# Performance work log

Measured on AMD Instinct MI355X. Metric: run time of the kernel, lower is better.

## Reference

```python
import jax, jax.numpy as jnp
import numpy as np

N = 100000
E = 600000
H = 128
G = 64          # number of graphs
LN_EPS = 1e-5


def setup_inputs() -> dict:
    key = jax.random.key(0)
    ks = jax.random.split(key, 16)
    node = jax.random.normal(ks[0], (N, H), dtype=jnp.float32)
    edge_index = jax.random.randint(ks[1], (2, E), 0, N, dtype=jnp.int64)
    edge_attr = jax.random.normal(ks[2], (E, 1), dtype=jnp.float32)
    batch_ptr = jnp.sort(jax.random.randint(ks[3], (N,), 0, G, dtype=jnp.int64))
    s = 1.0 / np.sqrt(H)
    params = dict(
        eps=jnp.float32(0.0),  # GINConv train_eps=True, init 0
        W1=jax.random.uniform(ks[4], (H, H), jnp.float32, -s, s),
        b1=jnp.zeros((H,), jnp.float32),
        g1=jnp.ones((H,), jnp.float32), be1=jnp.zeros((H,), jnp.float32),
        W2=jax.random.uniform(ks[5], (H, H), jnp.float32, -s, s),
        b2=jnp.zeros((H,), jnp.float32),
        g2=jnp.ones((H,), jnp.float32), be2=jnp.zeros((H,), jnp.float32),
        W3=jax.random.uniform(ks[6], (H, H), jnp.float32, -s, s),
        b3=jnp.zeros((H,), jnp.float32),
        ln_w=jnp.ones((H,), jnp.float32), ln_b=jnp.zeros((H,), jnp.float32),
    )
    return dict(node=node, edge_index=edge_index, edge_attr=edge_attr,
                batch_ptr=batch_ptr, **params)


def _layernorm(x, g, b):
    mu = x.mean(-1, keepdims=True)
    var = ((x - mu) ** 2).mean(-1, keepdims=True)
    return (x - mu) * jax.lax.rsqrt(var + LN_EPS) * g + b


def _forward(node, edge_index, batch_ptr, eps, W1, b1, g1, be1, W2, b2, g2, be2,
             W3, b3, ln_w, ln_b):
    src, dst = edge_index[0], edge_index[1]
    # GIN sum aggregation: scatter-add neighbor features to targets
    agg = jax.ops.segment_sum(node[src], dst, num_segments=N)  # [N, H]
    h = (1.0 + eps) * node + agg
    # 3-layer MLP (PyG MLP: lin -> LayerNorm -> ReLU, final lin plain)
    h = jax.nn.relu(_layernorm(h @ W1 + b1, g1, be1))
    h = jax.nn.relu(_layernorm(h @ W2 + b2, g2, be2))
    h = h @ W3 + b3
    # PyG graph-mode LayerNorm: normalize over all nodes+features per graph
    cnt = jax.ops.segment_sum(jnp.ones((N,), h.dtype), batch_ptr, num_segments=G)
    norm = jnp.maximum(cnt * H, 1.0)                       # [G]
    mean = jax.ops.segment_sum(h.sum(-1), batch_ptr, num_segments=G) / norm
    hc = h - mean[batch_ptr][:, None]
    var = jax.ops.segment_sum((hc * hc).sum(-1), batch_ptr, num_segments=G) / norm
    out = hc * jax.lax.rsqrt(var + LN_EPS)[batch_ptr][:, None] * ln_w + ln_b
    return jax.nn.relu(out)


def reference(node, edge_index, edge_attr, batch_ptr, eps, W1, b1, g1, be1,
              W2, b2, g2, be2, W3, b3, ln_w, ln_b):
    del edge_attr  # accepted by GIN_Layer.forward but unused
    return _forward(node, edge_index, batch_ptr, eps, W1, b1, g1, be1,
                    W2, b2, g2, be2, W3, b3, ln_w, ln_b)
```

## Files before the change

### kernel.cpp

```cpp
#include <hip/hip_runtime.h>

#define N_NODES 100000
#define N_EDGES 600000
#define H 128
#define G_NUM 64
#define LN_EPS 1e-5f

#define WSTR 136

#define NTILES ((N_NODES + 63) / 64)

#define SCAN_CHUNK 1024
#define SCAN_NB ((N_NODES + SCAN_CHUNK - 1) / SCAN_CHUNK)
#define HIST_NB ((N_EDGES + 255) / 256)
#define CVT_NB ((N_NODES * H / 8 + 255) / 256)
#define FILL_NB ((N_EDGES + 255) / 256)
#define WT_NB ((3 * 16384 + 255) / 256)

#define SCR_MAX 272

#define WT_IOFF 900612
#define NBF_IOFF 925192
#define NEEDED_WS ((size_t)NBF_IOFF * 4 + (size_t)N_NODES * H * 2)

typedef __attribute__((ext_vector_type(8))) short short8;
typedef __attribute__((ext_vector_type(4))) float floatx4;

__device__ __forceinline__ unsigned short f2bf(float x) {
    unsigned int u = __float_as_uint(x);
    u += 0x7fffu + ((u >> 16) & 1u);
    return (unsigned short)(u >> 16);
}

__global__ __launch_bounds__(256) void hist_cvt_kernel(
    const int* __restrict__ ei, int* __restrict__ deg,
    const float* __restrict__ node, unsigned int* __restrict__ node_bf)
{
    int gb = blockIdx.x;
    if (gb < HIST_NB) {
        int e = gb * 256 + threadIdx.x;
        if (e >= N_EDGES) return;
        atomicAdd(&deg[ei[N_EDGES + e]], 1);
    } else {
        int i = (gb - HIST_NB) * 256 + threadIdx.x;
        if (i >= N_NODES * H / 8) return;
        float4 a = ((const float4*)node)[i * 2];
        float4 b = ((const float4*)node)[i * 2 + 1];
        uint4 p;
        p.x = (unsigned)f2bf(a.x) | ((unsigned)f2bf(a.y) << 16);
        p.y = (unsigned)f2bf(a.z) | ((unsigned)f2bf(a.w) << 16);
        p.z = (unsigned)f2bf(b.x) | ((unsigned)f2bf(b.y) << 16);
        p.w = (unsigned)f2bf(b.z) | ((unsigned)f2bf(b.w) << 16);
        ((uint4*)node_bf)[i] = p;
    }
}

__global__ __launch_bounds__(256) void scan1_kernel(
    const int* __restrict__ deg, int* __restrict__ off,
    int* __restrict__ blksum)
{
    __shared__ int sA[256], sB[256];
    const int tid = threadIdx.x;
    const int base = blockIdx.x * SCAN_CHUNK + tid * 4;
    int v[4];
#pragma unroll
    for (int j = 0; j < 4; ++j) {
        int i = base + j;
        v[j] = (i < N_NODES) ? deg[i] : 0;
    }
    int tsum = v[0] + v[1] + v[2] + v[3];
    int* a = sA; int* b = sB;
    a[tid] = tsum;
    __syncthreads();
#pragma unroll
    for (int o = 1; o < 256; o <<= 1) {
        int t = a[tid] + ((tid >= o) ? a[tid - o] : 0);
        b[tid] = t;
        __syncthreads();
        int* tmp = a; a = b; b = tmp;
    }
    int run = a[tid] - tsum;
#pragma unroll
    for (int j = 0; j < 4; ++j) {
        int i = base + j;
        if (i < N_NODES) off[i] = run;
        run += v[j];
    }
    if (tid == 255) blksum[blockIdx.x] = a[255];
}

__global__ __launch_bounds__(256) void scan23_kernel(
    int* __restrict__ off, const int* __restrict__ blksum,
    int* __restrict__ cursor)
{
    __shared__ int sA[128], sB[128];
    const int tid = threadIdx.x;
    if (tid < 128) sA[tid] = (tid < SCAN_NB) ? blksum[tid] : 0;
    __syncthreads();
    int* a = sA; int* b = sB;
#pragma unroll
    for (int o = 1; o < 128; o <<= 1) {
        int t = 0;
        if (tid < 128) t = a[tid] + ((tid >= o) ? a[tid - o] : 0);
        __syncthreads();
        if (tid < 128) b[tid] = t;
        __syncthreads();
        int* tmp = a; a = b; b = tmp;
    }
    int excl = 0;
    if (tid < 128) excl = a[tid] - ((tid < SCAN_NB) ? blksum[tid] : 0);
    __syncthreads();
    if (tid < 128) sA[tid] = excl;
    __syncthreads();

    int i = blockIdx.x * 256 + tid;
    if (i < N_NODES) {
        int val = off[i] + sA[i >> 10];
        off[i] = val;
        cursor[i] = val;
    }
    if (i == 0) off[N_NODES] = N_EDGES;
}

__global__ __launch_bounds__(256) void fill_wt_kernel(
    const int* __restrict__ ei, int* __restrict__ cursor,
    int* __restrict__ csr,
    const float* __restrict__ W1, const float* __restrict__ W2,
    const float* __restrict__ W3, unsigned short* __restrict__ WT)
{
    int gb = blockIdx.x;
    if (gb < FILL_NB) {
        int e = gb * 256 + threadIdx.x;
        if (e >= N_EDGES) return;
        int dst = ei[N_EDGES + e];
        int pos = atomicAdd(&cursor[dst], 1);
        csr[pos] = ei[e];
    } else {
        int idx = (gb - FILL_NB) * 256 + threadIdx.x;
        if (idx >= 3 * 16384) return;
        int l = idx >> 14, r = idx & 16383;
        int frag = r >> 3, j = r & 7;
        int lane = frag & 63, ktnt = frag >> 6;
        int kt = ktnt & 3, nt = ktnt >> 2;
        int c = lane & 15, q = lane >> 4;
        int n = nt * 16 + c;
        int k = kt * 32 + q * 8 + j;
        const float* W = (l == 0) ? W1 : ((l == 1) ? W2 : W3);
        WT[l * 16384 + r] = f2bf(W[k * 128 + n]);
    }
}

__device__ __forceinline__ void gemm_frags(const unsigned short* hIn,
                                           const unsigned short* __restrict__ WTl,
                                           floatx4 acc[8], int w, int lane)
{
    const int c = lane & 15, q = lane >> 4;
#pragma unroll
    for (int nt = 0; nt < 8; ++nt) acc[nt] = (floatx4){0.f, 0.f, 0.f, 0.f};
#pragma unroll
    for (int kt = 0; kt < 4; ++kt) {
        short8 a = *(const short8*)&hIn[(w * 16 + c) * WSTR + kt * 32 + q * 8];
#pragma unroll
        for (int nt = 0; nt < 8; ++nt) {
            short8 b = *(const short8*)&WTl[(nt * 256 + kt * 64 + lane) * 8];
            acc[nt] = __builtin_amdgcn_mfma_f32_16x16x32_bf16(a, b, acc[nt], 0, 0, 0);
        }
    }
}

__device__ __forceinline__ void gemm_layer_ln(unsigned short* h,
                                              const unsigned short* __restrict__ WTl,
                                              const float* __restrict__ bias,
                                              const float* __restrict__ g,
                                              const float* __restrict__ be,
                                              int w, int lane)
{
    const int c = lane & 15, q = lane >> 4;
    floatx4 acc[8];
    gemm_frags(h, WTl, acc, w, lane);

    float sum[4] = {0.f, 0.f, 0.f, 0.f};
    float sq[4]  = {0.f, 0.f, 0.f, 0.f};
#pragma unroll
    for (int nt = 0; nt < 8; ++nt) {
        float bv = bias[nt * 16 + c];
#pragma unroll
        for (int i = 0; i < 4; ++i) {
            float vv = acc[nt][i] + bv;
            acc[nt][i] = vv;
            sum[i] += vv; sq[i] += vv * vv;
        }
    }
#pragma unroll
    for (int m = 1; m < 16; m <<= 1) {
#pragma unroll
        for (int i = 0; i < 4; ++i) {
            sum[i] += __shfl_xor(sum[i], m);
            sq[i]  += __shfl_xor(sq[i], m);
        }
    }
    float mu[4], rstd[4];
#pragma unroll
    for (int i = 0; i < 4; ++i) {
        mu[i]   = sum[i] * (1.0f / 128.0f);
        rstd[i] = rsqrtf(sq[i] * (1.0f / 128.0f) - mu[i] * mu[i] + LN_EPS);
    }
#pragma unroll
    for (int nt = 0; nt < 8; ++nt) {
        float gw = g[nt * 16 + c];
        float bw = be[nt * 16 + c];
#pragma unroll
        for (int i = 0; i < 4; ++i) {
            float val = fmaxf(0.f, (acc[nt][i] - mu[i]) * rstd[i] * gw + bw);
            h[(w * 16 + q * 4 + i) * WSTR + nt * 16 + c] = f2bf(val);
        }
    }
}

template <bool NBF>
__global__ __launch_bounds__(256, 6) void fused_mlp_kernel(
    const float* __restrict__ node, const unsigned int* __restrict__ nbf,
    const int* __restrict__ off,
    const int* __restrict__ csr, const float* __restrict__ epsp,
    const unsigned short* __restrict__ WT,
    const float* __restrict__ b1, const float* __restrict__ g1,
    const float* __restrict__ be1,
    const float* __restrict__ b2, const float* __restrict__ g2,
    const float* __restrict__ be2,
    const float* __restrict__ b3, const int* __restrict__ batch,
    float* __restrict__ out, float* __restrict__ gstat)
{
    __shared__ unsigned short hA[64 * WSTR];
    __shared__ float prm[7 * 128];
    __shared__ float s_gsum[G_NUM], s_gsq[G_NUM], s_gcnt[G_NUM];

    const int tid = threadIdx.x;
    const int w = tid >> 6, lane = tid & 63;
    const int row0 = blockIdx.x * 64;

    if (tid < G_NUM) { s_gsum[tid] = 0.f; s_gsq[tid] = 0.f; s_gcnt[tid] = 0.f; }
    {
        const float* srcs[7] = {b1, g1, be1, b2, g2, be2, b3};
#pragma unroll
        for (int t = 0; t < 4; ++t) {
            int i = tid + t * 256;
            if (i < 7 * 128) prm[i] = srcs[i >> 7][i & 127];
        }
    }

    {
        const float2* np2 = (const float2*)node;
        const float epsv = 1.0f + epsp[0];

        auto ld = [&](int n) -> float2 {
            if constexpr (NBF) {
                unsigned int u = nbf[(size_t)n * 64 + lane];
                return make_float2(__uint_as_float(u << 16),
                                   __uint_as_float(u & 0xffff0000u));
            } else {
                return np2[(size_t)n * 64 + lane];
            }
        };

        const int n0 = row0 + w * 16;
        int oidx = n0 + ((lane < 17) ? lane : 16);
        if (oidx > N_NODES) oidx = N_NODES;
        const int offl = off[oidx];
        const int e_begin = __shfl(offl, 0);
        const int e_end   = __shfl(offl, 16);
        const int cnt = e_end - e_begin;

        unsigned short* band = &hA[(w * 16) * WSTR];

        if (cnt <= SCR_MAX) {
            int* scr = ((int*)band) + (1088 - cnt);
            for (int k = lane; k < cnt; k += 64) scr[k] = csr[e_begin + k];
            __threadfence_block();

#pragma unroll
            for (int g4 = 0; g4 < 4; ++g4) {
                int p[4], e[4];
#pragma unroll
                for (int j = 0; j < 4; ++j) {
                    p[j] = __shfl(offl, g4 * 4 + j) - e_begin;
                    e[j] = __shfl(offl, g4 * 4 + j + 1) - e_begin;
                }
                float2 acc[4];
#pragma unroll
                for (int j = 0; j < 4; ++j) {
                    int n = n0 + g4 * 4 + j;
                    if (n < N_NODES) {
                        float2 own = ld(n);
                        acc[j] = make_float2(epsv * own.x, epsv * own.y);
                    } else {
                        acc[j] = make_float2(0.f, 0.f);
                    }
                }
                bool a0[4], a1[4];
                float2 b0[4], b1[4];
#pragma unroll
                for (int j = 0; j < 4; ++j) {
                    a0[j] = p[j] < e[j];
                    b0[j] = make_float2(0.f, 0.f);
                    if (a0[j]) {
                        int nb = __builtin_amdgcn_readfirstlane(scr[p[j]]);
                        b0[j] = ld(nb);
                    }
                }
#pragma unroll
                for (int j = 0; j < 4; ++j) {
                    a1[j] = (p[j] + 1) < e[j];
                    b1[j] = make_float2(0.f, 0.f);
                    if (a1[j]) {
                        int nb = __builtin_amdgcn_readfirstlane(scr[p[j] + 1]);
                        b1[j] = ld(nb);
                    }
                }
                while (a0[0] || a0[1] || a0[2] || a0[3]) {
                    float2 b2[4]; bool a2[4];
#pragma unroll
                    for (int j = 0; j < 4; ++j) {
                        a2[j] = (p[j] + 2) < e[j];
                        b2[j] = make_float2(0.f, 0.f);
                        if (a2[j]) {
                            int nb = __builtin_amdgcn_readfirstlane(scr[p[j] + 2]);
                            b2[j] = ld(nb);
                        }
                    }
#pragma unroll
                    for (int j = 0; j < 4; ++j) {
                        if (a0[j]) {
                            acc[j].x += b0[j].x; acc[j].y += b0[j].y;
                            p[j] += 1;
                        }
                        a0[j] = a1[j]; b0[j] = b1[j];
                        a1[j] = a2[j]; b1[j] = b2[j];
                    }
                }
#pragma unroll
                for (int j = 0; j < 4; ++j) {
                    unsigned int pk = (unsigned)f2bf(acc[j].x) |
                                      ((unsigned)f2bf(acc[j].y) << 16);
                    ((unsigned int*)&band[(g4 * 4 + j) * WSTR])[lane] = pk;
                }
            }
        } else {
#pragma unroll
            for (int g4 = 0; g4 < 4; ++g4) {
                float2 acc[4];
#pragma unroll
                for (int j = 0; j < 4; ++j) {
                    int n = n0 + g4 * 4 + j;
                    if (n < N_NODES) {
                        float2 own = ld(n);
                        acc[j] = make_float2(epsv * own.x, epsv * own.y);
                    } else {
                        acc[j] = make_float2(0.f, 0.f);
                    }
                }
                for (int j = 0; j < 4; ++j) {
                    int n = n0 + g4 * 4 + j;
                    if (n >= N_NODES) continue;
                    for (int t = off[n]; t < off[n + 1]; ++t) {
                        float2 v = ld(csr[t]);
                        acc[j].x += v.x; acc[j].y += v.y;
                    }
                }
#pragma unroll
                for (int j = 0; j < 4; ++j) {
                    unsigned int pk = (unsigned)f2bf(acc[j].x) |
                                      ((unsigned)f2bf(acc[j].y) << 16);
                    ((unsigned int*)&band[(g4 * 4 + j) * WSTR])[lane] = pk;
                }
            }
        }
    }
    __syncthreads();

    gemm_layer_ln(hA, WT,         &prm[0],   &prm[128], &prm[256], w, lane);
    gemm_layer_ln(hA, WT + 16384, &prm[384], &prm[512], &prm[640], w, lane);

    {
        const int c = lane & 15, q = lane >> 4;
        floatx4 acc3[8];
        gemm_frags(hA, WT + 32768, acc3, w, lane);
        float sum[4] = {0.f, 0.f, 0.f, 0.f};
        float sq[4]  = {0.f, 0.f, 0.f, 0.f};
#pragma unroll
        for (int nt = 0; nt < 8; ++nt) {
            float bv = prm[768 + nt * 16 + c];
#pragma unroll
            for (int i = 0; i < 4; ++i) {
                float vv = acc3[nt][i] + bv;
                size_t nrow = (size_t)row0 + w * 16 + q * 4 + i;
                if (nrow < N_NODES)
                    out[nrow * H + nt * 16 + c] = vv;
                sum[i] += vv; sq[i] += vv * vv;
            }
        }
#pragma unroll
        for (int m = 1; m < 16; m <<= 1) {
#pragma unroll
            for (int i = 0; i < 4; ++i) {
                sum[i] += __shfl_xor(sum[i], m);
                sq[i]  += __shfl_xor(sq[i], m);
            }
        }
        if (c == 0) {
#pragma unroll
            for (int i = 0; i < 4; ++i) {
                size_t nrow = (size_t)row0 + w * 16 + q * 4 + i;
                if (nrow < N_NODES) {
                    int g = batch[nrow];
                    atomicAdd(&s_gsum[g], sum[i]);
                    atomicAdd(&s_gsq[g], sq[i]);
                    atomicAdd(&s_gcnt[g], 1.0f);
                }
            }
        }
    }
    __syncthreads();
    if (tid < G_NUM && s_gcnt[tid] > 0.f) {
        unsafeAtomicAdd(&gstat[tid], s_gsum[tid]);
        unsafeAtomicAdd(&gstat[G_NUM + tid], s_gsq[tid]);
        unsafeAtomicAdd(&gstat[2 * G_NUM + tid], s_gcnt[tid]);
    }
}

__global__ __launch_bounds__(256) void final_ln_kernel(
    float* __restrict__ h3, const int* __restrict__ batch,
    const float* __restrict__ lnw, const float* __restrict__ lnb,
    const float* __restrict__ gstat)
{
    int idx4 = blockIdx.x * 256 + threadIdx.x;
    if (idx4 >= N_NODES * 32) return;
    int node = idx4 >> 5;
    int c4 = (idx4 & 31) * 4;
    int g = batch[node];
    float s   = gstat[g];
    float qq  = gstat[G_NUM + g];
    float cnt = gstat[2 * G_NUM + g];
    float norm = fmaxf(cnt * (float)H, 1.0f);
    float mean = s / norm;
    float var  = qq / norm - mean * mean;
    float inv  = rsqrtf(var + LN_EPS);
    float4 v = ((const float4*)h3)[idx4];
    float4 w = *(const float4*)&lnw[c4];
    float4 b = *(const float4*)&lnb[c4];
    v.x = fmaxf(0.f, (v.x - mean) * inv * w.x + b.x);
    v.y = fmaxf(0.f, (v.y - mean) * inv * w.y + b.y);
    v.z = fmaxf(0.f, (v.z - mean) * inv * w.z + b.z);
    v.w = fmaxf(0.f, (v.w - mean) * inv * w.w + b.w);
    ((float4*)h3)[idx4] = v;
}

extern "C" void kernel_launch(void* const* d_in, const int* in_sizes, int n_in,
                              void* d_out, int out_size, void* d_ws, size_t ws_size,
                              hipStream_t stream)
{
    const float* node  = (const float*)d_in[0];
    const int*   ei    = (const int*)d_in[1];
    const int*   batch = (const int*)d_in[3];
    const float* epsp  = (const float*)d_in[4];
    const float* W1    = (const float*)d_in[5];
    const float* b1    = (const float*)d_in[6];
    const float* g1    = (const float*)d_in[7];
    const float* be1   = (const float*)d_in[8];
    const float* W2    = (const float*)d_in[9];
    const float* b2    = (const float*)d_in[10];
    const float* g2    = (const float*)d_in[11];
    const float* be2   = (const float*)d_in[12];
    const float* W3    = (const float*)d_in[13];
    const float* b3    = (const float*)d_in[14];
    const float* lnw   = (const float*)d_in[15];
    const float* lnb   = (const float*)d_in[16];

    float* out = (float*)d_out;

    int* base = (int*)d_ws;
    float* gstat  = (float*)d_ws;
    int*   deg    = base + 512;
    int*   off    = deg + N_NODES;
    int*   cursor = off + N_NODES + 1;
    int*   csr    = cursor + N_NODES;
    int*   blksum = csr + N_EDGES;
    unsigned short* WT = (unsigned short*)(base + WT_IOFF);
    unsigned int*  nbf = (unsigned int*)(base + NBF_IOFF);

    const bool use_bf = (ws_size >= NEEDED_WS);

    hipMemsetAsync(d_ws, 0, (512 + N_NODES) * sizeof(int), stream);

    hist_cvt_kernel<<<HIST_NB + (use_bf ? CVT_NB : 0), 256, 0, stream>>>(
        ei, deg, node, nbf);
    scan1_kernel<<<SCAN_NB, 256, 0, stream>>>(deg, off, blksum);
    scan23_kernel<<<(N_NODES + 255) / 256, 256, 0, stream>>>(off, blksum, cursor);
    fill_wt_kernel<<<FILL_NB + WT_NB, 256, 0, stream>>>(ei, cursor, csr,
                                                        W1, W2, W3, WT);

    if (use_bf)
        fused_mlp_kernel<true><<<NTILES, 256, 0, stream>>>(
            node, nbf, off, csr, epsp, WT, b1, g1, be1, b2, g2, be2, b3, batch,
            out, gstat);
    else
        fused_mlp_kernel<false><<<NTILES, 256, 0, stream>>>(
            node, nbf, off, csr, epsp, WT, b1, g1, be1, b2, g2, be2, b3, batch,
            out, gstat);

    final_ln_kernel<<<(N_NODES * 32 + 255) / 256, 256, 0, stream>>>(
        out, batch, lnw, lnb, gstat);
}
```

Measured before the change: 358.4 us.

## Split fused gather+MLP kernel into separate gather and MLP kernels

```diff
diff --git a/kernel.cpp b/kernel.cpp
--- a/kernel.cpp
+++ b/kernel.cpp
@@ -19,9 +19,11 @@
 
 #define SCR_MAX 272
 
-#define WT_IOFF 900612
-#define NBF_IOFF 925192
-#define NEEDED_WS ((size_t)NBF_IOFF * 4 + (size_t)N_NODES * H * 2)
+#define WT_IOFF   900612
+#define NBF_IOFF  925192
+#define H0_BF_IOFF (NBF_IOFF + N_NODES * (H / 2))
+#define NEEDED_MIN ((size_t)(NBF_IOFF + N_NODES * (H / 2)) * 4)
+#define NEEDED_BF  ((size_t)(H0_BF_IOFF + N_NODES * (H / 2)) * 4)
 
 typedef __attribute__((ext_vector_type(8))) short short8;
 typedef __attribute__((ext_vector_type(4))) float floatx4;
@@ -150,6 +152,148 @@
     }
 }
 
+template <bool NBF>
+__global__ __launch_bounds__(256) void gather_kernel(
+    const float* __restrict__ node, const unsigned int* __restrict__ nbf,
+    const int* __restrict__ off, const int* __restrict__ csr,
+    const float* __restrict__ epsp, unsigned int* __restrict__ h0)
+{
+    __shared__ int scr4[4][SCR_MAX];
+    const int tid = threadIdx.x;
+    const int w = tid >> 6, lane = tid & 63;
+    const int n0 = blockIdx.x * 64 + w * 16;
+
+    const float2* np2 = (const float2*)node;
+    const float epsv = 1.0f + epsp[0];
+
+    auto ld = [&](int n) -> float2 {
+        if constexpr (NBF) {
+            unsigned int u = nbf[(size_t)n * 64 + lane];
+            return make_float2(__uint_as_float(u << 16),
+                               __uint_as_float(u & 0xffff0000u));
+        } else {
+            return np2[(size_t)n * 64 + lane];
+        }
+    };
+
+    int oidx = n0 + ((lane < 17) ? lane : 16);
+    if (oidx > N_NODES) oidx = N_NODES;
+    const int offl = off[oidx];
+    const int e_begin = __shfl(offl, 0);
+    const int e_end   = __shfl(offl, 16);
+    const int cnt = e_end - e_begin;
+
+    int* scr = scr4[w];
+
+    if (cnt <= SCR_MAX) {
+        for (int k = lane; k < cnt; k += 64) scr[k] = csr[e_begin + k];
+        __threadfence_block();
+
+#pragma unroll
+        for (int g4 = 0; g4 < 4; ++g4) {
+            int p[4], e[4];
+#pragma unroll
+            for (int j = 0; j < 4; ++j) {
+                p[j] = __shfl(offl, g4 * 4 + j) - e_begin;
+                e[j] = __shfl(offl, g4 * 4 + j + 1) - e_begin;
+            }
+            float2 acc[4];
+#pragma unroll
+            for (int j = 0; j < 4; ++j) {
+                int n = n0 + g4 * 4 + j;
+                if (n < N_NODES) {
+                    float2 own = ld(n);
+                    acc[j] = make_float2(epsv * own.x, epsv * own.y);
+                } else {
+                    acc[j] = make_float2(0.f, 0.f);
+                }
+            }
+            bool a0[4], a1[4];
+            float2 b0[4], b1[4];
+#pragma unroll
+            for (int j = 0; j < 4; ++j) {
+                a0[j] = p[j] < e[j];
+                b0[j] = make_float2(0.f, 0.f);
+                if (a0[j]) {
+                    int nb = __builtin_amdgcn_readfirstlane(scr[p[j]]);
+                    b0[j] = ld(nb);
+                }
+            }
+#pragma unroll
+            for (int j = 0; j < 4; ++j) {
+                a1[j] = (p[j] + 1) < e[j];
+                b1[j] = make_float2(0.f, 0.f);
+                if (a1[j]) {
+                    int nb = __builtin_amdgcn_readfirstlane(scr[p[j] + 1]);
+                    b1[j] = ld(nb);
+                }
+            }
+            while (a0[0] || a0[1] || a0[2] || a0[3]) {
+                float2 b2[4]; bool a2[4];
+#pragma unroll
+                for (int j = 0; j < 4; ++j) {
+                    a2[j] = (p[j] + 2) < e[j];
+                    b2[j] = make_float2(0.f, 0.f);
+                    if (a2[j]) {
+                        int nb = __builtin_amdgcn_readfirstlane(scr[p[j] + 2]);
+                        b2[j] = ld(nb);
+                    }
+                }
+#pragma unroll
+                for (int j = 0; j < 4; ++j) {
+                    if (a0[j]) {
+                        acc[j].x += b0[j].x; acc[j].y += b0[j].y;
+                        p[j] += 1;
+                    }
+                    a0[j] = a1[j]; b0[j] = b1[j];
+                    a1[j] = a2[j]; b1[j] = b2[j];
+                }
+            }
+#pragma unroll
+            for (int j = 0; j < 4; ++j) {
+                int n = n0 + g4 * 4 + j;
+                if (n < N_NODES) {
+                    unsigned int pk = (unsigned)f2bf(acc[j].x) |
+                                      ((unsigned)f2bf(acc[j].y) << 16);
+                    h0[(size_t)n * 64 + lane] = pk;
+                }
+            }
+        }
+    } else {
+#pragma unroll
+        for (int g4 = 0; g4 < 4; ++g4) {
+            float2 acc[4];
+#pragma unroll
+            for (int j = 0; j < 4; ++j) {
+                int n = n0 + g4 * 4 + j;
+                if (n < N_NODES) {
+                    float2 own = ld(n);
+                    acc[j] = make_float2(epsv * own.x, epsv * own.y);
+                } else {
+                    acc[j] = make_float2(0.f, 0.f);
+                }
+            }
+            for (int j = 0; j < 4; ++j) {
+                int n = n0 + g4 * 4 + j;
+                if (n >= N_NODES) continue;
+                for (int t = off[n]; t < off[n + 1]; ++t) {
+                    float2 v = ld(csr[t]);
+                    acc[j].x += v.x; acc[j].y += v.y;
+                }
+            }
+#pragma unroll
+            for (int j = 0; j < 4; ++j) {
+                int n = n0 + g4 * 4 + j;
+                if (n < N_NODES) {
+                    unsigned int pk = (unsigned)f2bf(acc[j].x) |
+                                      ((unsigned)f2bf(acc[j].y) << 16);
+                    h0[(size_t)n * 64 + lane] = pk;
+                }
+            }
+        }
+    }
+}
+
 __device__ __forceinline__ void gemm_frags(const unsigned short* hIn,
                                            const unsigned short* __restrict__ WTl,
                                            floatx4 acc[8], int w, int lane)
@@ -217,11 +361,8 @@
     }
 }
 
-template <bool NBF>
-__global__ __launch_bounds__(256, 6) void fused_mlp_kernel(
-    const float* __restrict__ node, const unsigned int* __restrict__ nbf,
-    const int* __restrict__ off,
-    const int* __restrict__ csr, const float* __restrict__ epsp,
+__global__ __launch_bounds__(256) void mlp_kernel(
+    const unsigned int* __restrict__ h0,
     const unsigned short* __restrict__ WT,
     const float* __restrict__ b1, const float* __restrict__ g1,
     const float* __restrict__ be1,
@@ -249,130 +390,18 @@
     }
 
     {
-        const float2* np2 = (const float2*)node;
-        const float epsv = 1.0f + epsp[0];
-
-        auto ld = [&](int n) -> float2 {
-            if constexpr (NBF) {
-                unsigned int u = nbf[(size_t)n * 64 + lane];
-                return make_float2(__uint_as_float(u << 16),
-                                   __uint_as_float(u & 0xffff0000u));
-            } else {
-                return np2[(size_t)n * 64 + lane];
-            }
-        };
-
-        const int n0 = row0 + w * 16;
-        int oidx = n0 + ((lane < 17) ? lane : 16);
-        if (oidx > N_NODES) oidx = N_NODES;
-        const int offl = off[oidx];
-        const int e_begin = __shfl(offl, 0);
-        const int e_end   = __shfl(offl, 16);
-        const int cnt = e_end - e_begin;
-
-        unsigned short* band = &hA[(w * 16) * WSTR];
-
-        if (cnt <= SCR_MAX) {
-            int* scr = ((int*)band) + (1088 - cnt);
-            for (int k = lane; k < cnt; k += 64) scr[k] = csr[e_begin + k];
-            __threadfence_block();
-
-#pragma unroll
-            for (int g4 = 0; g4 < 4; ++g4) {
-                int p[4], e[4];
-#pragma unroll
-                for (int j = 0; j < 4; ++j) {
-                    p[j] = __shfl(offl, g4 * 4 + j) - e_begin;
-                    e[j] = __shfl(offl, g4 * 4 + j + 1) - e_begin;
-                }
-                float2 acc[4];
-#pragma unroll
-                for (int j = 0; j < 4; ++j) {
-                    int n = n0 + g4 * 4 + j;
-                    if (n < N_NODES) {
-                        float2 own = ld(n);
-                        acc[j] = make_float2(epsv * own.x, epsv * own.y);
-                    } else {
-                        acc[j] = make_float2(0.f, 0.f);
-                    }
-                }
-                bool a0[4], a1[4];
-                float2 b0[4], b1[4];
-#pragma unroll
-                for (int j = 0; j < 4; ++j) {
-                    a0[j] = p[j] < e[j];
-                    b0[j] = make_float2(0.f, 0.f);
-                    if (a0[j]) {
-                        int nb = __builtin_amdgcn_readfirstlane(scr[p[j]]);
-                        b0[j] = ld(nb);
-                    }
-                }
-#pragma unroll
-                for (int j = 0; j < 4; ++j) {
-                    a1[j] = (p[j] + 1) < e[j];
-                    b1[j] = make_float2(0.f, 0.f);
-                    if (a1[j]) {
-                        int nb = __builtin_amdgcn_readfirstlane(scr[p[j] + 1]);
-                        b1[j] = ld(nb);
-                    }
-                }
-                while (a0[0] || a0[1] || a0[2] || a0[3]) {
-                    float2 b2[4]; bool a2[4];
-#pragma unroll
-                    for (int j = 0; j < 4; ++j) {
-                        a2[j] = (p[j] + 2) < e[j];
-                        b2[j] = make_float2(0.f, 0.f);
-                        if (a2[j]) {
-                            int nb = __builtin_amdgcn_readfirstlane(scr[p[j] + 2]);
-                            b2[j] = ld(nb);
-                        }
-                    }
-#pragma unroll
-                    for (int j = 0; j < 4; ++j) {
-                        if (a0[j]) {
-                            acc[j].x += b0[j].x; acc[j].y += b0[j].y;
-                            p[j] += 1;
-                        }
-                        a0[j] = a1[j]; b0[j] = b1[j];
-                        a1[j] = a2[j]; b1[j] = b2[j];
-                    }
-                }
-#pragma unroll
-                for (int j = 0; j < 4; ++j) {
-                    unsigned int pk = (unsigned)f2bf(acc[j].x) |
-                                      ((unsigned)f2bf(acc[j].y) << 16);
-                    ((unsigned int*)&band[(g4 * 4 + j) * WSTR])[lane] = pk;
-                }
-            }
+        const int r = tid >> 2;
+        const int q4 = tid & 3;
+        uint4* d = (uint4*)(((unsigned int*)hA) + r * (WSTR / 2) + q4 * 16);
+        const int row = row0 + r;
+        if (row < N_NODES) {
+            const uint4* s = (const uint4*)&h0[(size_t)row * 64 + q4 * 16];
+#pragma unroll
+            for (int k = 0; k < 4; ++k) d[k] = s[k];
         } else {
-#pragma unroll
-            for (int g4 = 0; g4 < 4; ++g4) {
-                float2 acc[4];
-#pragma unroll
-                for (int j = 0; j < 4; ++j) {
-                    int n = n0 + g4 * 4 + j;
-                    if (n < N_NODES) {
-                        float2 own = ld(n);
-                        acc[j] = make_float2(epsv * own.x, epsv * own.y);
-                    } else {
-                        acc[j] = make_float2(0.f, 0.f);
-                    }
-                }
-                for (int j = 0; j < 4; ++j) {
-                    int n = n0 + g4 * 4 + j;
-                    if (n >= N_NODES) continue;
-                    for (int t = off[n]; t < off[n + 1]; ++t) {
-                        float2 v = ld(csr[t]);
-                        acc[j].x += v.x; acc[j].y += v.y;
-                    }
-                }
-#pragma unroll
-                for (int j = 0; j < 4; ++j) {
-                    unsigned int pk = (unsigned)f2bf(acc[j].x) |
-                                      ((unsigned)f2bf(acc[j].y) << 16);
-                    ((unsigned int*)&band[(g4 * 4 + j) * WSTR])[lane] = pk;
-                }
-            }
+            uint4 z = make_uint4(0, 0, 0, 0);
+#pragma unroll
+            for (int k = 0; k < 4; ++k) d[k] = z;
         }
     }
     __syncthreads();
@@ -485,9 +514,11 @@
     int*   csr    = cursor + N_NODES;
     int*   blksum = csr + N_EDGES;
     unsigned short* WT = (unsigned short*)(base + WT_IOFF);
-    unsigned int*  nbf = (unsigned int*)(base + NBF_IOFF);
-
-    const bool use_bf = (ws_size >= NEEDED_WS);
+
+    const bool use_bf = (ws_size >= NEEDED_BF);
+    unsigned int* nbf = (unsigned int*)(base + NBF_IOFF);
+    unsigned int* h0  = use_bf ? (unsigned int*)(base + H0_BF_IOFF)
+                               : (unsigned int*)(base + NBF_IOFF);
 
     hipMemsetAsync(d_ws, 0, (512 + N_NODES) * sizeof(int), stream);
 
@@ -499,13 +530,14 @@
                                                         W1, W2, W3, WT);
 
     if (use_bf)
-        fused_mlp_kernel<true><<<NTILES, 256, 0, stream>>>(
-            node, nbf, off, csr, epsp, WT, b1, g1, be1, b2, g2, be2, b3, batch,
-            out, gstat);
+        gather_kernel<true><<<NTILES, 256, 0, stream>>>(node, nbf, off, csr,
+                                                        epsp, h0);
     else
-        fused_mlp_kernel<false><<<NTILES, 256, 0, stream>>>(
-            node, nbf, off, csr, epsp, WT, b1, g1, be1, b2, g2, be2, b3, batch,
-            out, gstat);
+        gather_kernel<false><<<NTILES, 256, 0, stream>>>(node, nbf, off, csr,
+                                                         epsp, h0);
+
+    mlp_kernel<<<NTILES, 256, 0, stream>>>(h0, WT, b1, g1, be1, b2, g2, be2,
+                                           b3, batch, out, gstat);
 
     final_ln_kernel<<<(N_NODES * 32 + 255) / 256, 256, 0, stream>>>(
         out, batch, lnw, lnb, gstat);
```

Result: faster. 344.5 us (-3.9%).
